# Optimization experiments

Hardware: AMD Instinct MI355X
Metric: run time of the kernel (lower is better)

The kernel has to match this reference:

```python
import jax, jax.numpy as jnp
import numpy as np
from jax import lax

DIM = 256
HEADS = 8
EPS = 1e-12  # torch F.normalize eps


def setup_inputs() -> dict:
    key = jax.random.key(0)
    ks = jax.random.split(key, 6)
    b, c, h, w = 2, DIM, 128, 128
    x = jax.random.normal(ks[0], (b, c, h, w), dtype=jnp.float32)
    # qkv 1x1 conv (no bias): weight [3*dim, dim]
    w_qkv = jax.random.normal(ks[1], (3 * c, c), dtype=jnp.float32) * (1.0 / np.sqrt(c))
    # depthwise 3x3 conv, groups = 3*dim: weight [3*dim, 1, 3, 3]
    w_dw = jax.random.normal(ks[2], (3 * c, 1, 3, 3), dtype=jnp.float32) * (1.0 / 3.0)
    # project_out 1x1 conv: [dim, dim]
    w_proj = jax.random.normal(ks[3], (c, c), dtype=jnp.float32) * (1.0 / np.sqrt(c))
    temperature = jnp.ones((HEADS, 1, 1), dtype=jnp.float32)
    a1 = jnp.full((1,), 0.2, dtype=jnp.float32)
    a2 = jnp.full((1,), 0.2, dtype=jnp.float32)
    a3 = jnp.full((1,), 0.2, dtype=jnp.float32)
    a4 = jnp.full((1,), 0.2, dtype=jnp.float32)
    return {"x": x, "w_qkv": w_qkv, "w_dw": w_dw, "w_proj": w_proj,
            "temperature": temperature, "a1": a1, "a2": a2, "a3": a3, "a4": a4}


def _l2norm(t):
    # torch F.normalize(dim=-1): t / max(||t||, eps)
    n = jnp.sqrt(jnp.sum(t * t, axis=-1, keepdims=True))
    return t / jnp.maximum(n, EPS)


def reference(x, w_qkv, w_dw, w_proj, temperature, a1, a2, a3, a4):
    b, c, h, w = x.shape
    heads = temperature.shape[0]
    C = c // heads
    hw = h * w
    # 1x1 conv then depthwise 3x3 conv (groups = 3c)
    qkv = jnp.einsum('oc,bchw->bohw', w_qkv, x)
    qkv = lax.conv_general_dilated(
        qkv, w_dw, window_strides=(1, 1), padding='SAME',
        dimension_numbers=('NCHW', 'OIHW', 'NCHW'), feature_group_count=3 * c)
    q, k, v = jnp.split(qkv, 3, axis=1)
    q = _l2norm(q.reshape(b, heads, C, hw))
    k = _l2norm(k.reshape(b, heads, C, hw))
    v = v.reshape(b, heads, C, hw)
    # channel attention: [b, heads, C, C]
    attn = jnp.einsum('bhcn,bhdn->bhcd', q, k) * temperature
    flat = attn.reshape(b, heads, C * C)
    # share one descending sort across all four top-k passes
    sorted_desc = jnp.sort(flat, axis=-1)[..., ::-1]
    N = C * C
    neg_inf = jnp.asarray(-jnp.inf, dtype=flat.dtype)

    def spar_softmax(topk):
        thresh = sorted_desc[..., topk - 1:topk]  # kth largest value
        masked = jnp.where(flat >= thresh, flat, neg_inf)
        return jax.nn.softmax(masked, axis=-1).reshape(b, heads, C, C)

    s1 = spar_softmax(N * 1 // 2)
    s2 = spar_softmax(N * 2 // 3)
    s3 = spar_softmax(N * 3 // 4)
    s4 = spar_softmax(N * 4 // 5)
    spar = s1 * a1 + s2 * a2 + s3 * a3 + s4 * a4
    out = jnp.einsum('bhcd,bhdn->bhcn', spar, v).reshape(b, c, h, w)
    out = jnp.einsum('oc,bchw->bohw', w_proj, out)
    return out
```

## Files before the change

### kernel.cpp

```cpp
#include <hip/hip_runtime.h>
#include <stdint.h>

#define HW     16384
#define IMGW   128
#define NCH    768
#define DIMC   256
#define NB     2
#define CPH    32

typedef unsigned short u16;
typedef unsigned int   u32;
typedef __attribute__((ext_vector_type(8))) short bf16x8;
typedef __attribute__((ext_vector_type(4))) float f32x4;

__device__ __forceinline__ float bf2f(u16 u) { return __uint_as_float(((u32)u) << 16); }
__device__ __forceinline__ u16 f2bf(float f) {
    u32 u = __float_as_uint(f);
    u += 0x7fffu + ((u >> 16) & 1u);
    return (u16)(u >> 16);
}

#define GLOAD16(gp, lp) __builtin_amdgcn_global_load_lds( \
    (const __attribute__((address_space(1))) void*)(gp),  \
    (__attribute__((address_space(3))) void*)(lp), 16, 0, 0)

__global__ __launch_bounds__(256)
void wsplit(const float* __restrict__ w, u16* __restrict__ wh, u16* __restrict__ wl)
{
    const int idx = blockIdx.x * 256 + threadIdx.x;
    const int m = idx >> 3, s = idx & 7;
    const int p = (m >> 1) & 3;
    #pragma unroll
    for (int u = 0; u < 4; ++u) {
        const int cb = s * 32 + ((u ^ p) << 3);
        u32 hq[4], lq[4];
        #pragma unroll
        for (int e2 = 0; e2 < 4; ++e2) {
            float f0 = w[m * 256 + cb + 2 * e2];
            float f1 = w[m * 256 + cb + 2 * e2 + 1];
            u16 h0 = f2bf(f0); u16 l0 = f2bf(f0 - bf2f(h0));
            u16 h1 = f2bf(f1); u16 l1 = f2bf(f1 - bf2f(h1));
            hq[e2] = (u32)h0 | ((u32)h1 << 16);
            lq[e2] = (u32)l0 | ((u32)l1 << 16);
        }
        size_t rowb = ((size_t)(s * 768 + m)) << 6;
        uint4 hv = {hq[0], hq[1], hq[2], hq[3]};
        uint4 lv = {lq[0], lq[1], lq[2], lq[3]};
        *(uint4*)((char*)wh + rowb + (u << 4)) = hv;
        *(uint4*)((char*)wl + rowb + (u << 4)) = lv;
    }
}

__global__ __launch_bounds__(256)
void transp_split(const float* __restrict__ src, long srcBatch,
                  u16* __restrict__ dsth, u16* __restrict__ dstl)
{
    __shared__ float Xs[64][68];
    const int bz = blockIdx.y;
    const int nt = blockIdx.x & 255;
    const int ct = blockIdx.x >> 8;
    const int n0 = nt * 64, c0 = ct * 64;
    const int t = threadIdx.x;
    const float* xb = src + (size_t)bz * srcBatch;

    #pragma unroll
    for (int it = 0; it < 4; ++it) {
        int cl = (t >> 4) + it * 16;
        int nl4 = (t & 15) << 2;
        float4 v = *(const float4*)(xb + (size_t)(c0 + cl) * HW + n0 + nl4);
        Xs[cl][nl4]     = v.x; Xs[cl][nl4 + 1] = v.y;
        Xs[cl][nl4 + 2] = v.z; Xs[cl][nl4 + 3] = v.w;
    }
    __syncthreads();

    const int nl = t >> 2, u = t & 3;
    const int p = (nl >> 1) & 3;
    #pragma unroll
    for (int sl = 0; sl < 2; ++sl) {
        const int s = (c0 >> 5) + sl;
        const int cb = sl * 32 + ((u ^ p) << 3);
        u32 hq[4], lq[4];
        #pragma unroll
        for (int e2 = 0; e2 < 4; ++e2) {
            float f0 = Xs[cb + 2 * e2][nl];
            float f1 = Xs[cb + 2 * e2 + 1][nl];
            u16 h0 = f2bf(f0); u16 l0 = f2bf(f0 - bf2f(h0));
            u16 h1 = f2bf(f1); u16 l1 = f2bf(f1 - bf2f(h1));
            hq[e2] = (u32)h0 | ((u32)h1 << 16);
            lq[e2] = (u32)l0 | ((u32)l1 << 16);
        }
        size_t rowb = ((size_t)((bz * 8 + s)) * 16384 + n0 + nl) << 6;
        uint4 hv = {hq[0], hq[1], hq[2], hq[3]};
        uint4 lv = {lq[0], lq[1], lq[2], lq[3]};
        *(uint4*)((char*)dsth + rowb + (u << 4)) = hv;
        *(uint4*)((char*)dstl + rowb + (u << 4)) = lv;
    }
}

template<bool FULLB, bool OUTBF16, int MBLKS>
__global__ __launch_bounds__(256, 2)
void gemm_mfma_split(const u16* __restrict__ Ahp, const u16* __restrict__ Alp,
                     const u16* __restrict__ Bhp, const u16* __restrict__ Blp,
                     void* __restrict__ Cp, int aBatch, int aSlice, long cBatch)
{
    constexpr int BUFSZ = FULLB ? 32768 : 24576;
    __shared__ char smem[2 * BUFSZ];

    const int t    = threadIdx.x;
    const int lane = t & 63;
    const int w    = t >> 6;
    const int per = gridDim.x >> 3;
    const int wid = (blockIdx.x & 7) * per + (blockIdx.x >> 3);
    const int nglob = wid / MBLKS;
    const int m0 = (wid % MBLKS) * 128;
    const int bz = nglob >> 7;
    const int n0 = (nglob & 127) * 128;

    const int lrow  = lane >> 2;
    const int lquad = lane & 3;
    const int mh = w >> 1, nh = w & 1;
    const int swz = ((lane & 15) << 6) + ((((lane >> 4) ^ ((lane >> 1) & 3))) << 4);

    f32x4 acc[4][4];
    #pragma unroll
    for (int i = 0; i < 4; ++i)
        #pragma unroll
        for (int j = 0; j < 4; ++j)
            acc[i][j] = (f32x4){0.f, 0.f, 0.f, 0.f};

    auto stage = [&](int buf, int s) {
        const size_t arow0 = (size_t)bz * aBatch + (size_t)s * aSlice + m0;
        const size_t brow0 = ((size_t)(bz * 8 + s)) * 16384 + n0;
        char* base = smem + buf * BUFSZ;
        constexpr int NCHK = FULLB ? 8 : 6;
        #pragma unroll
        for (int i = 0; i < NCHK; ++i) {
            const int tile = i >> 1;
            const int r16  = ((i & 1) << 2) | w;
            char* dst = base + tile * 8192 + r16 * 1024;
            const char* src;
            if (tile == 0)
                src = (const char*)Ahp + ((arow0 + r16 * 16 + lrow) << 6) + (lquad << 4);
            else if (tile == 1)
                src = (const char*)Alp + ((arow0 + r16 * 16 + lrow) << 6) + (lquad << 4);
            else if (tile == 2)
                src = (const char*)Bhp + ((brow0 + r16 * 16 + lrow) << 6) + (lquad << 4);
            else
                src = (const char*)Blp + ((brow0 + r16 * 16 + lrow) << 6) + (lquad << 4);
            GLOAD16(src, dst);
        }
    };

    stage(0, 0);
    __syncthreads();

    #pragma unroll
    for (int s = 0; s < 8; ++s) {
        char* base = smem + (s & 1) * BUFSZ;
        if (s < 7) stage((s + 1) & 1, s + 1);

        bf16x8 ah[4], al[4], bh[4], bl[4];
        #pragma unroll
        for (int f = 0; f < 4; ++f) {
            const int aoff = (mh * 64 + f * 16) * 64 + swz;
            ah[f] = *(const bf16x8*)(base + aoff);
            al[f] = *(const bf16x8*)(base + 8192 + aoff);
            const int boff = (nh * 64 + f * 16) * 64 + swz;
            bh[f] = *(const bf16x8*)(base + 16384 + boff);
            if (FULLB) bl[f] = *(const bf16x8*)(base + 24576 + boff);
        }

        #pragma unroll
        for (int fm = 0; fm < 4; ++fm)
            #pragma unroll
            for (int fn = 0; fn < 4; ++fn) {
                acc[fm][fn] = __builtin_amdgcn_mfma_f32_16x16x32_bf16(ah[fm], bh[fn], acc[fm][fn], 0, 0, 0);
                if (FULLB)
                    acc[fm][fn] = __builtin_amdgcn_mfma_f32_16x16x32_bf16(ah[fm], bl[fn], acc[fm][fn], 0, 0, 0);
                acc[fm][fn] = __builtin_amdgcn_mfma_f32_16x16x32_bf16(al[fm], bh[fn], acc[fm][fn], 0, 0, 0);
            }

        if (s < 7) __syncthreads();
    }

    #pragma unroll
    for (int fm = 0; fm < 4; ++fm) {
        const int mrow0 = m0 + mh * 64 + fm * 16 + ((lane >> 4) << 2);
        #pragma unroll
        for (int fn = 0; fn < 4; ++fn) {
            const int ncol = n0 + nh * 64 + fn * 16 + (lane & 15);
            if (OUTBF16) {
                u16* Cb = (u16*)Cp + (size_t)bz * cBatch;
                #pragma unroll
                for (int r = 0; r < 4; ++r)
                    Cb[(size_t)(mrow0 + r) * HW + ncol] = f2bf(acc[fm][fn][r]);
            } else {
                float* Cb = (float*)Cp + (size_t)bz * cBatch;
                #pragma unroll
                for (int r = 0; r < 4; ++r)
                    Cb[(size_t)(mrow0 + r) * HW + ncol] = acc[fm][fn][r];
            }
        }
    }
}

__global__ __launch_bounds__(256)
void dwconv_all(const u16* __restrict__ qkvb, const float* __restrict__ wdw,
                u16* __restrict__ dwb, u16* __restrict__ vth)
{
    __shared__ u16 Lout[256][40];
    const int bid = blockIdx.x;
    const int t = threadIdx.x;

    if (bid < 1024) {
        const int rp = bid & 63;
        const int s  = (bid >> 6) & 7;
        const int bz = bid >> 9;
        const int ch = t >> 3;
        const int cg = t & 7;
        const int r0 = rp * 2;
        const int c0 = cg * 16;
        const int chg = 512 + s * 32 + ch;
        const u16* plane = qkvb + ((size_t)bz * NCH + chg) * HW;
        const float* wp = wdw + chg * 9;
        float w[9];
        #pragma unroll
        for (int i = 0; i < 9; ++i) w[i] = wp[i];

        float rv[4][18];
        #pragma unroll
        for (int j = 0; j < 4; ++j) {
            const int ry = r0 - 1 + j;
            if (ry < 0 || ry >= IMGW) {
                #pragma unroll
                for (int k = 0; k < 18; ++k) rv[j][k] = 0.f;
            } else {
                const u16* rw = plane + ry * IMGW;
                bf16x8 v0 = *(const bf16x8*)(rw + c0);
                bf16x8 v1 = *(const bf16x8*)(rw + c0 + 8);
                u32 lw = (u32)__shfl_up((int)(u16)v1[7], 1);
                u32 rr = (u32)__shfl_down((int)(u16)v0[0], 1);
                rv[j][0] = (c0 > 0) ? bf2f((u16)lw) : 0.f;
                #pragma unroll
                for (int e = 0; e < 8; ++e) {
                    rv[j][1 + e] = bf2f((u16)v0[e]);
                    rv[j][9 + e] = bf2f((u16)v1[e]);
                }
                rv[j][17] = (c0 < 112) ? bf2f((u16)rr) : 0.f;
            }
        }

        #pragma unroll
        for (int rr2 = 0; rr2 < 2; ++rr2) {
            float acc[16];
            #pragma unroll
            for (int q = 0; q < 16; ++q) acc[q] = 0.f;
            #pragma unroll
            for (int dy = 0; dy < 3; ++dy)
                #pragma unroll
                for (int dx = 0; dx < 3; ++dx) {
                    float wv = w[dy * 3 + dx];
                    #pragma unroll
                    for (int q = 0; q < 16; ++q)
                        acc[q] = fmaf(rv[rr2 + dy][q + dx], wv, acc[q]);
                }
            #pragma unroll
            for (int q = 0; q < 16; ++q)
                Lout[rr2 * 128 + c0 + q][ch] = f2bf(acc[q]);
        }
        __syncthreads();

        u16* dst = vth + (((size_t)(bz * 8 + s)) * 16384 + rp * 256 + t) * 32;
        const int pq = (t >> 1) & 3;
        #pragma unroll
        for (int u = 0; u < 4; ++u)
            *(uint4*)(dst + u * 8) = *(const uint4*)(&Lout[t][(u ^ pq) * 8]);
    } else {
        const int qid = bid - 1024;
        const int y  = qid >> 2;
        const int bi = y >> 9, ch = y & 511;
        const size_t p = (size_t)bi * NCH + ch;
        const int r0 = (qid & 3) * 32 + (t >> 5) * 4;
        const int c0 = (t & 31) << 2;

        const u16* plane = qkvb + p * HW;
        const float* wp = wdw + ch * 9;
        float w[9];
        #pragma unroll
        for (int i = 0; i < 9; ++i) w[i] = wp[i];

        float rv[6][6];
        #pragma unroll
        for (int j = 0; j < 6; ++j) {
            const int ry = r0 - 1 + j;
            if (ry < 0 || ry >= IMGW) {
                #pragma unroll
                for (int k = 0; k < 6; ++k) rv[j][k] = 0.f;
            } else {
                const u16* rp_ = plane + ry * IMGW;
                ushort4 vm = *(const ushort4*)(rp_ + c0);
                u32 lw = (u32)__shfl_up((int)vm.w, 1);
                u32 rr = (u32)__shfl_down((int)vm.x, 1);
                rv[j][0] = (c0 > 0)   ? bf2f((u16)lw) : 0.f;
                rv[j][1] = bf2f(vm.x); rv[j][2] = bf2f(vm.y);
                rv[j][3] = bf2f(vm.z); rv[j][4] = bf2f(vm.w);
                rv[j][5] = (c0 < 124) ? bf2f((u16)rr) : 0.f;
            }
        }

        #pragma unroll
        for (int rr2 = 0; rr2 < 4; ++rr2) {
            float acc[4] = {0.f, 0.f, 0.f, 0.f};
            #pragma unroll
            for (int dy = 0; dy < 3; ++dy) {
                #pragma unroll
                for (int dx = 0; dx < 3; ++dx) {
                    float wv = w[dy * 3 + dx];
                    #pragma unroll
                    for (int q = 0; q < 4; ++q)
                        acc[q] = fmaf(rv[rr2 + dy][q + dx], wv, acc[q]);
                }
            }
            ushort4 o4;
            o4.x = f2bf(acc[0]); o4.y = f2bf(acc[1]);
            o4.z = f2bf(acc[2]); o4.w = f2bf(acc[3]);
            *(ushort4*)(dwb + p * HW + (r0 + rr2) * IMGW + c0) = o4;
        }
    }
}

__global__ __launch_bounds__(256)
void gram_mfma(const u16* __restrict__ dw, float* __restrict__ part,
               float* __restrict__ sumsqp)
{
    __shared__ float pl[4][32][32];
    __shared__ float sl[4][64];
    const int chunk = blockIdx.x;
    const int bh    = blockIdx.y;
    const int bi = bh >> 3, h = bh & 7;
    const u16* qbase = dw + ((size_t)bi * NCH + h * CPH) * HW;
    const u16* kbase = dw + ((size_t)bi * NCH + 256 + h * CPH) * HW;
    const int t = threadIdx.x, lane = t & 63, w = t >> 6;
    const int lr = lane & 15;
    const int lg = lane >> 4;

    f32x4 acc[2][2];
    #pragma unroll
    for (int i = 0; i < 2; ++i)
        #pragma unroll
        for (int j = 0; j < 2; ++j)
            acc[i][j] = (f32x4){0.f, 0.f, 0.f, 0.f};
    float sq[4] = {0.f, 0.f, 0.f, 0.f};

    #pragma unroll
    for (int ks = 0; ks < 4; ++ks) {
        const int nb = chunk * 512 + w * 128 + ks * 32 + lg * 8;
        bf16x8 a0 = *(const bf16x8*)(qbase + (size_t)lr * HW + nb);
        bf16x8 a1 = *(const bf16x8*)(qbase + (size_t)(lr + 16) * HW + nb);
        bf16x8 b0 = *(const bf16x8*)(kbase + (size_t)lr * HW + nb);
        bf16x8 b1 = *(const bf16x8*)(kbase + (size_t)(lr + 16) * HW + nb);
        acc[0][0] = __builtin_amdgcn_mfma_f32_16x16x32_bf16(a0, b0, acc[0][0], 0, 0, 0);
        acc[0][1] = __builtin_amdgcn_mfma_f32_16x16x32_bf16(a0, b1, acc[0][1], 0, 0, 0);
        acc[1][0] = __builtin_amdgcn_mfma_f32_16x16x32_bf16(a1, b0, acc[1][0], 0, 0, 0);
        acc[1][1] = __builtin_amdgcn_mfma_f32_16x16x32_bf16(a1, b1, acc[1][1], 0, 0, 0);
        #pragma unroll
        for (int e = 0; e < 8; ++e) {
            float f0 = bf2f((u16)a0[e]); sq[0] = fmaf(f0, f0, sq[0]);
            float f1 = bf2f((u16)a1[e]); sq[1] = fmaf(f1, f1, sq[1]);
            float f2 = bf2f((u16)b0[e]); sq[2] = fmaf(f2, f2, sq[2]);
            float f3 = bf2f((u16)b1[e]); sq[3] = fmaf(f3, f3, sq[3]);
        }
    }
    #pragma unroll
    for (int i = 0; i < 4; ++i) {
        sq[i] += __shfl_xor(sq[i], 16);
        sq[i] += __shfl_xor(sq[i], 32);
    }
    if (lane < 16) {
        sl[w][lane]      = sq[0];
        sl[w][16 + lane] = sq[1];
        sl[w][32 + lane] = sq[2];
        sl[w][48 + lane] = sq[3];
    }
    #pragma unroll
    for (int qt = 0; qt < 2; ++qt)
        #pragma unroll
        for (int kt = 0; kt < 2; ++kt)
            #pragma unroll
            for (int r = 0; r < 4; ++r)
                pl[w][qt * 16 + lg * 4 + r][kt * 16 + lr] = acc[qt][kt][r];
    __syncthreads();

    #pragma unroll
    for (int i = 0; i < 4; ++i) {
        const int o = i * 256 + t;
        const int qc = o >> 5, kd = o & 31;
        float s = pl[0][qc][kd] + pl[1][qc][kd] + pl[2][qc][kd] + pl[3][qc][kd];
        part[((size_t)chunk * 16 + bh) * 1024 + o] = s;
    }
    if (t < 64) {
        float s = sl[0][t] + sl[1][t] + sl[2][t] + sl[3][t];
        sumsqp[((size_t)chunk * 16 + bh) * 64 + t] = s;
    }
}

__global__ __launch_bounds__(256)
void gram_finish(const float* __restrict__ part, const float* __restrict__ sumsqp,
                 const float* __restrict__ temp, float* __restrict__ attn)
{
    const int idx = blockIdx.x * 256 + threadIdx.x;
    const int bh = idx >> 10;
    const int h = bh & 7;
    const int c = (idx >> 5) & 31, d = idx & 31;
    float s = 0.f, sqq = 0.f, sqk = 0.f;
    #pragma unroll
    for (int ch = 0; ch < 32; ++ch) {
        s   += part[(size_t)ch * 16384 + idx];
        sqq += sumsqp[((size_t)ch * 16 + bh) * 64 + c];
        sqk += sumsqp[((size_t)ch * 16 + bh) * 64 + 32 + d];
    }
    float iq = 1.f / fmaxf(sqrtf(sqq), 1e-12f);
    float ik = 1.f / fmaxf(sqrtf(sqk), 1e-12f);
    attn[idx] = s * iq * ik * temp[h];
}

__global__ __launch_bounds__(128)
void rank4(const float* __restrict__ attn, float* __restrict__ vthr_g)
{
    __shared__ float xs[1024];
    const int seg = blockIdx.x, bh = blockIdx.y;
    const int t = threadIdx.x;
    const float* row = attn + bh * 1024;

    *(float4*)(&xs[t * 8])     = *(const float4*)(row + t * 8);
    *(float4*)(&xs[t * 8 + 4]) = *(const float4*)(row + t * 8 + 4);
    __syncthreads();

    const float x = xs[seg * 128 + t];
    int g = 0, e = 0;
    const float4* xs4 = (const float4*)xs;
    for (int j = 0; j < 256; ++j) {
        float4 v = xs4[j];
        g += (v.x > x) + (v.y > x) + (v.z > x) + (v.w > x);
        e += (v.x == x) + (v.y == x) + (v.z == x) + (v.w == x);
    }
    if (g == 0) vthr_g[bh * 8 + 4] = x;
    const int topks[4] = {512, 682, 768, 819};
    #pragma unroll
    for (int kk = 0; kk < 4; ++kk)
        if (g <= topks[kk] - 1 && topks[kk] - 1 < g + e) vthr_g[bh * 8 + kk] = x;
}

__global__ __launch_bounds__(1024)
void apply_soft(const float* __restrict__ attn, const float* __restrict__ vthr_g,
                float* __restrict__ spar,
                const float* __restrict__ a1, const float* __restrict__ a2,
                const float* __restrict__ a3, const float* __restrict__ a4)
{
    __shared__ float red[16 * 4];
    __shared__ float ssh[4];
    const int bh = blockIdx.x, t = threadIdx.x;
    const float x = attn[bh * 1024 + t];
    float vthr[4];
    #pragma unroll
    for (int kk = 0; kk < 4; ++kk) vthr[kk] = vthr_g[bh * 8 + kk];
    const float m = vthr_g[bh * 8 + 4];

    float ex = expf(x - m);
    float v4[4];
    #pragma unroll
    for (int kk = 0; kk < 4; ++kk) v4[kk] = (x >= vthr[kk]) ? ex : 0.f;
    #pragma unroll
    for (int off = 32; off; off >>= 1)
        #pragma unroll
        for (int kk = 0; kk < 4; ++kk) v4[kk] += __shfl_down(v4[kk], off);
    const int lane = t & 63, wid = t >> 6;
    if (lane == 0) {
        #pragma unroll
        for (int kk = 0; kk < 4; ++kk) red[wid * 4 + kk] = v4[kk];
    }
    __syncthreads();
    if (t == 0) {
        float s0 = 0, s1 = 0, s2 = 0, s3 = 0;
        for (int ww = 0; ww < 16; ++ww) {
            s0 += red[ww * 4 + 0]; s1 += red[ww * 4 + 1];
            s2 += red[ww * 4 + 2]; s3 += red[ww * 4 + 3];
        }
        ssh[0] = s0; ssh[1] = s1; ssh[2] = s2; ssh[3] = s3;
    }
    __syncthreads();

    float av[4] = {*a1, *a2, *a3, *a4};
    float coef = 0.f;
    #pragma unroll
    for (int kk = 0; kk < 4; ++kk)
        if (x >= vthr[kk]) coef += av[kk] / ssh[kk];
    spar[bh * 1024 + t] = ex * coef;
}

__global__ __launch_bounds__(256)
void build_m2_split(const float* __restrict__ wproj, const float* __restrict__ spar,
                    u16* __restrict__ m2h, u16* __restrict__ m2l)
{
    const int idx = blockIdx.x * 256 + threadIdx.x;
    const int b = idx >> 16, o = (idx >> 8) & 255, hd = idx & 255;
    const int h = hd >> 5, d = hd & 31;
    const float* wrow = wproj + o * 256 + h * CPH;
    const float* sp = spar + (size_t)(b * 8 + h) * 1024 + d;
    float acc = 0.f;
    #pragma unroll 8
    for (int cc = 0; cc < 32; ++cc)
        acc = fmaf(wrow[cc], sp[cc * 32], acc);
    u16 hi = f2bf(acc);
    u16 lo = f2bf(acc - bf2f(hi));
    const int s = hd >> 5, cslot = hd & 31;
    const int qt = cslot >> 3, e = cslot & 7;
    const int p = (o >> 1) & 3;
    size_t pos = ((size_t)(b * 2048 + s * 256 + o) << 5) + ((qt ^ p) << 3) + e;
    m2h[pos] = hi;
    m2l[pos] = lo;
}

extern "C" void kernel_launch(void* const* d_in, const int* in_sizes, int n_in,
                              void* d_out, int out_size, void* d_ws, size_t ws_size,
                              hipStream_t stream)
{
    const float* x      = (const float*)d_in[0];
    const float* w_qkv  = (const float*)d_in[1];
    const float* w_dw   = (const float*)d_in[2];
    const float* w_proj = (const float*)d_in[3];
    const float* temp   = (const float*)d_in[4];
    const float* a1     = (const float*)d_in[5];
    const float* a2     = (const float*)d_in[6];
    const float* a3     = (const float*)d_in[7];
    const float* a4     = (const float*)d_in[8];

    float* ws = (float*)d_ws;
    u16* qkvb = (u16*)ws;
    u16* vth  = (u16*)(ws + 12582912);
    float* sumsqp = ws;
    float* part   = ws + 32768;
    float* attn   = ws + 557056;
    float* spar   = ws + 573440;
    float* vthr_g = ws + 589824;
    u16* m2h = (u16*)(ws + 589952);
    u16* m2l = m2h + 131072;
    float* r1 = ws + (size_t)25165824;
    u16* xth = (u16*)r1;
    u16* xtl = xth + (size_t)8388608;
    u16* whp = xtl + (size_t)8388608;
    u16* wlp = whp + (size_t)196608;
    u16* dwb = (u16*)r1;

    wsplit<<<24, 256, 0, stream>>>(w_qkv, whp, wlp);
    transp_split<<<dim3(1024, 2), 256, 0, stream>>>(x, (long)DIMC * HW, xth, xtl);
    gemm_mfma_split<true, true, 6><<<1536, 256, 0, stream>>>(
        whp, wlp, xth, xtl, qkvb, 0, 768, (long)NCH * HW);
    dwconv_all<<<5120, 256, 0, stream>>>(qkvb, w_dw, dwb, vth);
    gram_mfma<<<dim3(32, 16), 256, 0, stream>>>(dwb, part, sumsqp);
    gram_finish<<<64, 256, 0, stream>>>(part, sumsqp, temp, attn);
    rank4<<<dim3(8, 16), 128, 0, stream>>>(attn, vthr_g);
    apply_soft<<<16, 1024, 0, stream>>>(attn, vthr_g, spar, a1, a2, a3, a4);
    build_m2_split<<<512, 256, 0, stream>>>(w_proj, spar, m2h, m2l);
    gemm_mfma_split<false, false, 2><<<512, 256, 0, stream>>>(
        m2h, m2l, vth, nullptr, d_out, 2048, 256, (long)DIMC * HW);
}
```

Measured before the change: 125.5 us.

## Widen GEMM tiles to 128x256 and drop double-buffered LDS staging

Both split-bf16 GEMMs now use a 128x256 output tile per block, so each warp holds 4x8 accumulators. This halves the grid and reuses each A fragment across twice as many B columns. Double buffering is replaced by a single LDS buffer with load-sync-compute per K slice, which removes the overlap of the next slice's global loads with MFMA work. The larger accumulator set raises register pressure under launch_bounds(256,2), and serialized loads may expose memory latency.

After: 129.9 us. +3.4%, slower.

```diff
diff --git a/kernel.cpp b/kernel.cpp
--- a/kernel.cpp
+++ b/kernel.cpp
@@ -99,12 +99,12 @@
 
 template<bool FULLB, bool OUTBF16, int MBLKS>
 __global__ __launch_bounds__(256, 2)
-void gemm_mfma_split(const u16* __restrict__ Ahp, const u16* __restrict__ Alp,
-                     const u16* __restrict__ Bhp, const u16* __restrict__ Blp,
-                     void* __restrict__ Cp, int aBatch, int aSlice, long cBatch)
-{
-    constexpr int BUFSZ = FULLB ? 32768 : 24576;
-    __shared__ char smem[2 * BUFSZ];
+void gemm_big(const u16* __restrict__ Ahp, const u16* __restrict__ Alp,
+              const u16* __restrict__ Bhp, const u16* __restrict__ Blp,
+              void* __restrict__ Cp, int aBatch, int aSlice, long cBatch)
+{
+    constexpr int LDSSZ = FULLB ? 49152 : 32768;
+    __shared__ char smem[LDSSZ];
 
     const int t    = threadIdx.x;
     const int lane = t & 63;
@@ -113,82 +113,71 @@
     const int wid = (blockIdx.x & 7) * per + (blockIdx.x >> 3);
     const int nglob = wid / MBLKS;
     const int m0 = (wid % MBLKS) * 128;
-    const int bz = nglob >> 7;
-    const int n0 = (nglob & 127) * 128;
-
-    const int lrow  = lane >> 2;
-    const int lquad = lane & 3;
+    const int bz = nglob >> 6;
+    const int n0 = (nglob & 63) * 256;
+
     const int mh = w >> 1, nh = w & 1;
     const int swz = ((lane & 15) << 6) + ((((lane >> 4) ^ ((lane >> 1) & 3))) << 4);
-
-    f32x4 acc[4][4];
+    const int su = t & 3;
+    const int sr = t >> 2;
+
+    f32x4 acc[4][8];
     #pragma unroll
     for (int i = 0; i < 4; ++i)
         #pragma unroll
-        for (int j = 0; j < 4; ++j)
+        for (int j = 0; j < 8; ++j)
             acc[i][j] = (f32x4){0.f, 0.f, 0.f, 0.f};
 
-    auto stage = [&](int buf, int s) {
+    for (int s = 0; s < 8; ++s) {
         const size_t arow0 = (size_t)bz * aBatch + (size_t)s * aSlice + m0;
         const size_t brow0 = ((size_t)(bz * 8 + s)) * 16384 + n0;
-        char* base = smem + buf * BUFSZ;
-        constexpr int NCHK = FULLB ? 8 : 6;
+        if (s) __syncthreads();
+        constexpr int NCHK = FULLB ? 12 : 8;
         #pragma unroll
         for (int i = 0; i < NCHK; ++i) {
-            const int tile = i >> 1;
-            const int r16  = ((i & 1) << 2) | w;
-            char* dst = base + tile * 8192 + r16 * 1024;
+            char* dst = smem + i * 4096 + t * 16;
             const char* src;
-            if (tile == 0)
-                src = (const char*)Ahp + ((arow0 + r16 * 16 + lrow) << 6) + (lquad << 4);
-            else if (tile == 1)
-                src = (const char*)Alp + ((arow0 + r16 * 16 + lrow) << 6) + (lquad << 4);
-            else if (tile == 2)
-                src = (const char*)Bhp + ((brow0 + r16 * 16 + lrow) << 6) + (lquad << 4);
+            if (i < 2)
+                src = (const char*)Ahp + ((arow0 + i * 64 + sr) << 6) + (su << 4);
+            else if (i < 4)
+                src = (const char*)Alp + ((arow0 + (i - 2) * 64 + sr) << 6) + (su << 4);
+            else if (i < 8)
+                src = (const char*)Bhp + ((brow0 + (i - 4) * 64 + sr) << 6) + (su << 4);
             else
-                src = (const char*)Blp + ((brow0 + r16 * 16 + lrow) << 6) + (lquad << 4);
+                src = (const char*)Blp + ((brow0 + (i - 8) * 64 + sr) << 6) + (su << 4);
             GLOAD16(src, dst);
         }
-    };
-
-    stage(0, 0);
-    __syncthreads();
-
-    #pragma unroll
-    for (int s = 0; s < 8; ++s) {
-        char* base = smem + (s & 1) * BUFSZ;
-        if (s < 7) stage((s + 1) & 1, s + 1);
-
-        bf16x8 ah[4], al[4], bh[4], bl[4];
+        __syncthreads();
+
+        bf16x8 ah[4], al[4];
         #pragma unroll
         for (int f = 0; f < 4; ++f) {
             const int aoff = (mh * 64 + f * 16) * 64 + swz;
-            ah[f] = *(const bf16x8*)(base + aoff);
-            al[f] = *(const bf16x8*)(base + 8192 + aoff);
-            const int boff = (nh * 64 + f * 16) * 64 + swz;
-            bh[f] = *(const bf16x8*)(base + 16384 + boff);
-            if (FULLB) bl[f] = *(const bf16x8*)(base + 24576 + boff);
-        }
-
-        #pragma unroll
-        for (int fm = 0; fm < 4; ++fm)
+            ah[f] = *(const bf16x8*)(smem + aoff);
+            al[f] = *(const bf16x8*)(smem + 8192 + aoff);
+        }
+        #pragma unroll
+        for (int fn = 0; fn < 8; ++fn) {
+            const int boff = (nh * 128 + fn * 16) * 64 + swz;
+            bf16x8 bh = *(const bf16x8*)(smem + 16384 + boff);
+            bf16x8 bl;
+            if (FULLB) bl = *(const bf16x8*)(smem + 32768 + boff);
             #pragma unroll
-            for (int fn = 0; fn < 4; ++fn) {
-                acc[fm][fn] = __builtin_amdgcn_mfma_f32_16x16x32_bf16(ah[fm], bh[fn], acc[fm][fn], 0, 0, 0);
+            for (int fm = 0; fm < 4; ++fm) {
+                acc[fm][fn] = __builtin_amdgcn_mfma_f32_16x16x32_bf16(ah[fm], bh, acc[fm][fn], 0, 0, 0);
                 if (FULLB)
-                    acc[fm][fn] = __builtin_amdgcn_mfma_f32_16x16x32_bf16(ah[fm], bl[fn], acc[fm][fn], 0, 0, 0);
-                acc[fm][fn] = __builtin_amdgcn_mfma_f32_16x16x32_bf16(al[fm], bh[fn], acc[fm][fn], 0, 0, 0);
+                    acc[fm][fn] = __builtin_amdgcn_mfma_f32_16x16x32_bf16(ah[fm], bl, acc[fm][fn], 0, 0, 0);
+                acc[fm][fn] = __builtin_amdgcn_mfma_f32_16x16x32_bf16(al[fm], bh, acc[fm][fn], 0, 0, 0);
             }
-
-        if (s < 7) __syncthreads();
+        }
     }
 
     #pragma unroll
     for (int fm = 0; fm < 4; ++fm) {
         const int mrow0 = m0 + mh * 64 + fm * 16 + ((lane >> 4) << 2);
         #pragma unroll
-        for (int fn = 0; fn < 4; ++fn) {
-            const int ncol = n0 + nh * 64 + fn * 16 + (lane & 15);
+        for (int fn = 0; fn < 8; ++fn) {
+            const int ncol = n0 + nh * 128 + fn * 16 + (lane & 15);
             if (OUTBF16) {
                 u16* Cb = (u16*)Cp + (size_t)bz * cBatch;
                 #pragma unroll
@@ -554,7 +543,7 @@
 
     wsplit<<<24, 256, 0, stream>>>(w_qkv, whp, wlp);
     transp_split<<<dim3(1024, 2), 256, 0, stream>>>(x, (long)DIMC * HW, xth, xtl);
-    gemm_mfma_split<true, true, 6><<<1536, 256, 0, stream>>>(
+    gemm_big<true, true, 6><<<768, 256, 0, stream>>>(
         whp, wlp, xth, xtl, qkvb, 0, 768, (long)NCH * HW);
     dwconv_all<<<5120, 256, 0, stream>>>(qkvb, w_dw, dwb, vth);
     gram_mfma<<<dim3(32, 16), 256, 0, stream>>>(dwb, part, sumsqp);
@@ -562,6 +551,6 @@
     rank4<<<dim3(8, 16), 128, 0, stream>>>(attn, vthr_g);
     apply_soft<<<16, 1024, 0, stream>>>(attn, vthr_g, spar, a1, a2, a3, a4);
     build_m2_split<<<512, 256, 0, stream>>>(w_proj, spar, m2h, m2l);
-    gemm_mfma_split<false, false, 2><<<512, 256, 0, stream>>>(
+    gemm_big<false, false, 2><<<256, 256, 0, stream>>>(
         m2h, m2l, vth, nullptr, d_out, 2048, 256, (long)DIMC * HW);
 }
```
